# Kernel optimization log

Measured on AMD Instinct MI355X. Metric: run time of the kernel, lower is better.

## Reference

```python
import jax, jax.numpy as jnp
import numpy as np

R = 1.1
SCALE = 100.0
BUMP_STEPS = 32
NUM_THETAS = 32
NUM_FEATURES = 128
N_NODES = 200000
NUM_GRAPHS = 128


def setup_inputs() -> dict:
    key = jax.random.key(0)
    k1, k2, k3 = jax.random.split(key, 3)
    x = jax.random.normal(k1, (N_NODES, NUM_FEATURES), dtype=jnp.float32)
    batch = jnp.sort(jax.random.randint(k2, (N_NODES,), 0, NUM_GRAPHS, dtype=jnp.int64))
    v = jax.random.uniform(k3, (NUM_THETAS, NUM_FEATURES), dtype=jnp.float32) - 0.5
    return {"x": x, "batch": batch, "num_graphs": NUM_GRAPHS, "v": v}


def reference(x, batch, num_graphs, v):
    # nh: node heights along each direction theta -> [N, T]
    nh = x @ v.T
    # linspace over filtration values -> [S]
    lin = jnp.linspace(-R, R, BUMP_STEPS, dtype=nh.dtype)
    # bump: sigmoid difference; second point is the constant pad value R
    # ecc: [N, S, T]  (node-major so segment_sum reduces the leading axis)
    ecc = (jax.nn.sigmoid(SCALE * (lin[None, :, None] - nh[:, None, :]))
           - jax.nn.sigmoid(SCALE * (lin - R))[None, :, None])
    # scatter-add per graph label -> [ng, S, T] == index_add over dim1 then movedim(0,1)
    ect = jax.ops.segment_sum(ecc, batch, num_segments=num_graphs)
    return ect
```

## Files before the change

### kernel.cpp

```cpp
#include <hip/hip_runtime.h>
#include <math.h>

#define N_NODES 200000
#define NF 128
#define NT 32
#define NS 32
#define ATILE 64
#define ABLOCKS 3125
#define VSTRIDE 136
#define HPAD 33

typedef short bf16x8 __attribute__((ext_vector_type(8)));
typedef float floatx4 __attribute__((ext_vector_type(4)));

__device__ __forceinline__ float rcp_fast(float x) { return __builtin_amdgcn_rcpf(x); }

__device__ __forceinline__ void split_bf16(float f, unsigned short& h, unsigned short& l) {
    unsigned u  = __float_as_uint(f);
    unsigned r  = u + 0x7FFFu + ((u >> 16) & 1u);
    unsigned hb = r & 0xFFFF0000u;
    h = (unsigned short)(hb >> 16);
    float rem = f - __uint_as_float(hb);
    unsigned u2 = __float_as_uint(rem);
    unsigned r2 = u2 + 0x7FFFu + ((u2 >> 16) & 1u);
    l = (unsigned short)(r2 >> 16);
}

__device__ __forceinline__ void split8(float4 a, float4 b, bf16x8& h8, bf16x8& l8) {
    unsigned short h[8], l[8];
    split_bf16(a.x, h[0], l[0]); split_bf16(a.y, h[1], l[1]);
    split_bf16(a.z, h[2], l[2]); split_bf16(a.w, h[3], l[3]);
    split_bf16(b.x, h[4], l[4]); split_bf16(b.y, h[5], l[5]);
    split_bf16(b.z, h[6], l[6]); split_bf16(b.w, h[7], l[7]);
    h8 = (bf16x8){(short)h[0],(short)h[1],(short)h[2],(short)h[3],
                  (short)h[4],(short)h[5],(short)h[6],(short)h[7]};
    l8 = (bf16x8){(short)l[0],(short)l[1],(short)l[2],(short)l[3],
                  (short)l[4],(short)l[5],(short)l[6],(short)l[7]};
}

__device__ __forceinline__ void deposit(float* corr, int b, float z, float Lw, float C1) {
    float s0f = ceilf(z - 1.45f);
    int   s0  = (int)s0f;
    float e0  = __builtin_amdgcn_exp2f(Lw * (z - s0f));
    float e1  = e0 * C1;
    float e2  = e1 * C1;
    float f0  = rcp_fast(1.0f + e0);
    float f1  = rcp_fast(1.0f + e1);
    float f2  = rcp_fast(1.0f + e2);
    atomicAdd(&corr[b + max(s0, 0)], f0);
    int sB = max(s0 + 1, 0); if (sB < 32) atomicAdd(&corr[b + sB], f1 - f0);
    int sC = max(s0 + 2, 0); if (sC < 32) atomicAdd(&corr[b + sC], f2 - f1);
    int sD = s0 + 3;         if (sD < 32) atomicAdd(&corr[b + sD], 1.0f - f2);
}

__global__ __launch_bounds__(256, 7)
void ect_fused(const float* __restrict__ x,
               const int* __restrict__ batch,
               const float* __restrict__ v,
               float* __restrict__ out)
{
    __shared__ __align__(16) unsigned short vh[NT * VSTRIDE];
    __shared__ __align__(16) unsigned short vl[NT * VSTRIDE];
    __shared__ int   batch_lds[ATILE];
    __shared__ float corr[NT * HPAD];
    __shared__ float cnt_lds;

    const int tid  = threadIdx.x;
    const int blk  = blockIdx.x;
    const int w    = tid >> 6;
    const int lane = tid & 63;
    const int mrow = lane & 15;
    const int quad = lane >> 4;

    #pragma unroll
    for (int j = 0; j < 4; ++j) {
        int idx4 = j * 256 + tid;
        int row  = idx4 >> 5;
        int f4   = idx4 & 31;
        float4 val = *(const float4*)&v[(size_t)row * NF + f4 * 4];
        unsigned short h0,h1,h2,h3,l0,l1,l2,l3;
        split_bf16(val.x, h0, l0); split_bf16(val.y, h1, l1);
        split_bf16(val.z, h2, l2); split_bf16(val.w, h3, l3);
        uint2 hh, ll;
        hh.x = (unsigned)h0 | ((unsigned)h1 << 16); hh.y = (unsigned)h2 | ((unsigned)h3 << 16);
        ll.x = (unsigned)l0 | ((unsigned)l1 << 16); ll.y = (unsigned)l2 | ((unsigned)l3 << 16);
        *(uint2*)&vh[row * VSTRIDE + f4 * 4] = hh;
        *(uint2*)&vl[row * VSTRIDE + f4 * 4] = ll;
    }
    if (tid < ATILE) batch_lds[tid] = batch[blk * ATILE + tid];
    for (int i = tid; i < NT * HPAD; i += 256) corr[i] = 0.0f;

    const size_t arow = (size_t)blk * ATILE + w * 16 + mrow;
    const float* __restrict__ xrow = x + arow * NF + quad * 8;

    floatx4 acc0 = {0.f, 0.f, 0.f, 0.f};
    floatx4 acc1 = {0.f, 0.f, 0.f, 0.f};

    bf16x8 ah[4], al[4];
    #pragma unroll
    for (int slice = 0; slice < 4; ++slice) {
        float4 a0 = *(const float4*)&xrow[slice * 32];
        float4 a1 = *(const float4*)&xrow[slice * 32 + 4];
        split8(a0, a1, ah[slice], al[slice]);
    }
    __syncthreads();

    const int b0base = mrow * VSTRIDE + quad * 8;
    const int b1base = (16 + mrow) * VSTRIDE + quad * 8;
    #pragma unroll
    for (int slice = 0; slice < 4; ++slice) {
        bf16x8 bh0 = *(bf16x8*)&vh[b0base + slice * 32];
        bf16x8 bl0 = *(bf16x8*)&vl[b0base + slice * 32];
        bf16x8 bh1 = *(bf16x8*)&vh[b1base + slice * 32];
        bf16x8 bl1 = *(bf16x8*)&vl[b1base + slice * 32];
        acc0 = __builtin_amdgcn_mfma_f32_16x16x32_bf16(ah[slice], bh0, acc0, 0, 0, 0);
        acc0 = __builtin_amdgcn_mfma_f32_16x16x32_bf16(ah[slice], bl0, acc0, 0, 0, 0);
        acc0 = __builtin_amdgcn_mfma_f32_16x16x32_bf16(al[slice], bh0, acc0, 0, 0, 0);
        acc1 = __builtin_amdgcn_mfma_f32_16x16x32_bf16(ah[slice], bh1, acc1, 0, 0, 0);
        acc1 = __builtin_amdgcn_mfma_f32_16x16x32_bf16(ah[slice], bl1, acc1, 0, 0, 0);
        acc1 = __builtin_amdgcn_mfma_f32_16x16x32_bf16(al[slice], bh1, acc1, 0, 0, 0);
    }

    const float inv_dlin = 14.090909090909092f;
    const float Lw       = 10.23848093f;
    const float dlin     = 2.2f / 31.0f;
    const float L        = 144.26950408889634f;
    const float C1       = 8.2777115e-04f;

    const int g_first = batch_lds[0];
    const int g_last  = batch_lds[ATILE - 1];

    const int ft = tid & 31;
    const int sb = tid >> 5;
    float csk[4];
    #pragma unroll
    for (int k = 0; k < 4; ++k) {
        int s = sb + 8 * k;
        float lin_s = -1.1f + (float)s * dlin;
        csk[k] = rcp_fast(1.0f + __builtin_amdgcn_exp2f(L * (1.1f - lin_s)));
    }

    const int c0base = mrow * HPAD;
    const int c1base = (16 + mrow) * HPAD;

    for (int gp = g_first; gp <= g_last; ++gp) {
        if (tid < ATILE) {
            unsigned long long m = __ballot(batch_lds[tid] == gp);
            if (tid == 0) cnt_lds = (float)__popcll(m);
        }

        float c0 = 0.f, c1 = 0.f;
        #pragma unroll
        for (int reg = 0; reg < 4; ++reg) {
            const int n = w * 16 + quad * 4 + reg;
            if (batch_lds[n] == gp) {
                {
                    float z = fmaf(acc0[reg], inv_dlin, 15.5f);
                    if (z <= -1.45f)      c0 += 1.0f;
                    else if (z < 32.45f)  deposit(corr, c0base, z, Lw, C1);
                }
                {
                    float z = fmaf(acc1[reg], inv_dlin, 15.5f);
                    if (z <= -1.45f)      c1 += 1.0f;
                    else if (z < 32.45f)  deposit(corr, c1base, z, Lw, C1);
                }
            }
        }
        if (c0 != 0.f) atomicAdd(&corr[c0base], c0);
        if (c1 != 0.f) atomicAdd(&corr[c1base], c1);
        __syncthreads();

        {
            const int grp = tid >> 5;
            const int sc  = tid & 31;
            for (int row = grp; row < NT; row += 8) {
                float val = corr[row * HPAD + sc];
                #pragma unroll
                for (int d = 1; d < 32; d <<= 1) {
                    float nbr = __shfl_up(val, d, 32);
                    if (sc >= d) val += nbr;
                }
                corr[row * HPAD + sc] = val;
            }
        }
        __syncthreads();

        const float cnt = cnt_lds;
        #pragma unroll
        for (int k = 0; k < 4; ++k) {
            int s = sb + 8 * k;
            float val = corr[ft * HPAD + s] - cnt * csk[k];
            corr[ft * HPAD + s] = 0.0f;
            atomicAdd(&out[(size_t)gp * (NS * NT) + s * NT + ft], val);
        }
        if (gp < g_last) __syncthreads();
    }
}

extern "C" void kernel_launch(void* const* d_in, const int* in_sizes, int n_in,
                              void* d_out, int out_size, void* d_ws, size_t ws_size,
                              hipStream_t stream) {
    const float* x     = (const float*)d_in[0];
    const int*   batch = (const int*)d_in[1];
    const float* v     = (const float*)d_in[3];
    float*       out   = (float*)d_out;

    hipMemsetAsync(d_out, 0, (size_t)out_size * sizeof(float), stream);
    ect_fused<<<dim3(ABLOCKS), dim3(256), 0, stream>>>(x, batch, v, out);
}
```

Measured before the change: 207.4 us.

## Tile nodes per graph and reduce partial histograms instead of global atomics

```diff
diff --git a/kernel.cpp b/kernel.cpp
--- a/kernel.cpp
+++ b/kernel.cpp
@@ -5,8 +5,8 @@
 #define NF 128
 #define NT 32
 #define NS 32
-#define ATILE 64
-#define ABLOCKS 3125
+#define NG 128
+#define NTILES 30
 #define VSTRIDE 136
 #define HPAD 33
 
@@ -53,24 +53,50 @@
     int sD = s0 + 3;         if (sD < 32) atomicAdd(&corr[b + sD], 1.0f - f2);
 }
 
+__global__ __launch_bounds__(256)
+void graph_starts(const int* __restrict__ batch, int* __restrict__ starts) {
+    int i = blockIdx.x * 256 + threadIdx.x;
+    if (i >= N_NODES) return;
+    int b    = batch[i];
+    int prev = (i == 0) ? -1 : batch[i - 1];
+    for (int g = prev + 1; g <= b; ++g) starts[g] = i;
+    if (i == N_NODES - 1)
+        for (int g = b + 1; g <= NG; ++g) starts[g] = N_NODES;
+}
+
 __global__ __launch_bounds__(256, 7)
-void ect_fused(const float* __restrict__ x,
-               const int* __restrict__ batch,
-               const float* __restrict__ v,
-               float* __restrict__ out)
+void ect_tile(const float* __restrict__ x,
+              const float* __restrict__ v,
+              const int* __restrict__ starts,
+              float* __restrict__ partials,
+              float* __restrict__ out,
+              int use_ws)
 {
     __shared__ __align__(16) unsigned short vh[NT * VSTRIDE];
     __shared__ __align__(16) unsigned short vl[NT * VSTRIDE];
-    __shared__ int   batch_lds[ATILE];
     __shared__ float corr[NT * HPAD];
-    __shared__ float cnt_lds;
 
     const int tid  = threadIdx.x;
-    const int blk  = blockIdx.x;
+    const int t    = blockIdx.x;
+    const int g    = blockIdx.y;
     const int w    = tid >> 6;
     const int lane = tid & 63;
     const int mrow = lane & 15;
     const int quad = lane >> 4;
+
+    const int start = starts[g];
+    const int count = starts[g + 1] - start;
+    const int slot  = g * NTILES + t;
+
+    if (t * 64 >= count) {
+        if (use_ws) {
+            float4 z4 = {0.f, 0.f, 0.f, 0.f};
+            *(float4*)&partials[(size_t)slot * 1024 + tid * 4] = z4;
+        }
+        return;
+    }
+    const int base   = start + t * 64;
+    const int nvalid = min(64, count - t * 64);
 
     #pragma unroll
     for (int j = 0; j < 4; ++j) {
@@ -87,11 +113,10 @@
         *(uint2*)&vh[row * VSTRIDE + f4 * 4] = hh;
         *(uint2*)&vl[row * VSTRIDE + f4 * 4] = ll;
     }
-    if (tid < ATILE) batch_lds[tid] = batch[blk * ATILE + tid];
     for (int i = tid; i < NT * HPAD; i += 256) corr[i] = 0.0f;
 
-    const size_t arow = (size_t)blk * ATILE + w * 16 + mrow;
-    const float* __restrict__ xrow = x + arow * NF + quad * 8;
+    const int gi = min(base + w * 16 + mrow, N_NODES - 1);
+    const float* __restrict__ xrow = x + (size_t)gi * NF + quad * 8;
 
     floatx4 acc0 = {0.f, 0.f, 0.f, 0.f};
     floatx4 acc1 = {0.f, 0.f, 0.f, 0.f};
@@ -127,74 +152,76 @@
     const float L        = 144.26950408889634f;
     const float C1       = 8.2777115e-04f;
 
-    const int g_first = batch_lds[0];
-    const int g_last  = batch_lds[ATILE - 1];
-
-    const int ft = tid & 31;
-    const int sb = tid >> 5;
-    float csk[4];
-    #pragma unroll
-    for (int k = 0; k < 4; ++k) {
-        int s = sb + 8 * k;
-        float lin_s = -1.1f + (float)s * dlin;
-        csk[k] = rcp_fast(1.0f + __builtin_amdgcn_exp2f(L * (1.1f - lin_s)));
-    }
-
     const int c0base = mrow * HPAD;
     const int c1base = (16 + mrow) * HPAD;
 
-    for (int gp = g_first; gp <= g_last; ++gp) {
-        if (tid < ATILE) {
-            unsigned long long m = __ballot(batch_lds[tid] == gp);
-            if (tid == 0) cnt_lds = (float)__popcll(m);
-        }
-
-        float c0 = 0.f, c1 = 0.f;
-        #pragma unroll
-        for (int reg = 0; reg < 4; ++reg) {
-            const int n = w * 16 + quad * 4 + reg;
-            if (batch_lds[n] == gp) {
-                {
-                    float z = fmaf(acc0[reg], inv_dlin, 15.5f);
-                    if (z <= -1.45f)      c0 += 1.0f;
-                    else if (z < 32.45f)  deposit(corr, c0base, z, Lw, C1);
-                }
-                {
-                    float z = fmaf(acc1[reg], inv_dlin, 15.5f);
-                    if (z <= -1.45f)      c1 += 1.0f;
-                    else if (z < 32.45f)  deposit(corr, c1base, z, Lw, C1);
-                }
+    float c0 = 0.f, c1 = 0.f;
+    #pragma unroll
+    for (int reg = 0; reg < 4; ++reg) {
+        const int n = w * 16 + quad * 4 + reg;
+        if (n < nvalid) {
+            {
+                float z = fmaf(acc0[reg], inv_dlin, 15.5f);
+                if (z <= -1.45f)      c0 += 1.0f;
+                else if (z < 32.45f)  deposit(corr, c0base, z, Lw, C1);
+            }
+            {
+                float z = fmaf(acc1[reg], inv_dlin, 15.5f);
+                if (z <= -1.45f)      c1 += 1.0f;
+                else if (z < 32.45f)  deposit(corr, c1base, z, Lw, C1);
             }
         }
-        if (c0 != 0.f) atomicAdd(&corr[c0base], c0);
-        if (c1 != 0.f) atomicAdd(&corr[c1base], c1);
-        __syncthreads();
-
-        {
-            const int grp = tid >> 5;
-            const int sc  = tid & 31;
-            for (int row = grp; row < NT; row += 8) {
-                float val = corr[row * HPAD + sc];
-                #pragma unroll
-                for (int d = 1; d < 32; d <<= 1) {
-                    float nbr = __shfl_up(val, d, 32);
-                    if (sc >= d) val += nbr;
-                }
-                corr[row * HPAD + sc] = val;
+    }
+    if (c0 != 0.f) atomicAdd(&corr[c0base], c0);
+    if (c1 != 0.f) atomicAdd(&corr[c1base], c1);
+    __syncthreads();
+
+    {
+        const int grp = tid >> 5;
+        const int sc  = tid & 31;
+        for (int row = grp; row < NT; row += 8) {
+            float val = corr[row * HPAD + sc];
+            #pragma unroll
+            for (int d = 1; d < 32; d <<= 1) {
+                float nbr = __shfl_up(val, d, 32);
+                if (sc >= d) val += nbr;
             }
+            corr[row * HPAD + sc] = val;
         }
-        __syncthreads();
-
-        const float cnt = cnt_lds;
-        #pragma unroll
-        for (int k = 0; k < 4; ++k) {
-            int s = sb + 8 * k;
-            float val = corr[ft * HPAD + s] - cnt * csk[k];
-            corr[ft * HPAD + s] = 0.0f;
-            atomicAdd(&out[(size_t)gp * (NS * NT) + s * NT + ft], val);
-        }
-        if (gp < g_last) __syncthreads();
-    }
+    }
+    __syncthreads();
+
+    const float cnt  = (float)nvalid;
+    const int   s    = tid >> 3;
+    const int   ft0  = (tid & 7) * 4;
+    const float lin_s = -1.1f + (float)s * dlin;
+    const float cs    = rcp_fast(1.0f + __builtin_amdgcn_exp2f(L * (1.1f - lin_s)));
+    float4 r;
+    r.x = corr[(ft0 + 0) * HPAD + s] - cnt * cs;
+    r.y = corr[(ft0 + 1) * HPAD + s] - cnt * cs;
+    r.z = corr[(ft0 + 2) * HPAD + s] - cnt * cs;
+    r.w = corr[(ft0 + 3) * HPAD + s] - cnt * cs;
+    if (use_ws) {
+        *(float4*)&partials[(size_t)slot * 1024 + tid * 4] = r;
+    } else {
+        float* o = out + (size_t)g * (NS * NT) + tid * 4;
+        atomicAdd(&o[0], r.x); atomicAdd(&o[1], r.y);
+        atomicAdd(&o[2], r.z); atomicAdd(&o[3], r.w);
+    }
+}
+
+__global__ __launch_bounds__(256)
+void reduce_partials(const float* __restrict__ partials, float* __restrict__ out) {
+    const int g   = blockIdx.x;
+    const int tid = threadIdx.x;
+    const float4* p4 = (const float4*)partials;
+    float4 acc = {0.f, 0.f, 0.f, 0.f};
+    #pragma unroll
+    for (int t = 0; t < NTILES; ++t) {
+        float4 v = p4[(size_t)(g * NTILES + t) * 256 + tid];
+        acc.x += v.x; acc.y += v.y; acc.z += v.z; acc.w += v.w;
+    }
+    ((float4*)out)[(size_t)g * 256 + tid] = acc;
 }
 
 extern "C" void kernel_launch(void* const* d_in, const int* in_sizes, int n_in,
@@ -205,6 +232,14 @@
     const float* v     = (const float*)d_in[3];
     float*       out   = (float*)d_out;
 
+    int*   starts   = (int*)d_ws;
+    float* partials = (float*)((char*)d_ws + 1024);
+    const size_t need = 1024 + (size_t)NG * NTILES * 1024 * sizeof(float);
+    const int use_ws  = (ws_size >= need) ? 1 : 0;
+
     hipMemsetAsync(d_out, 0, (size_t)out_size * sizeof(float), stream);
-    ect_fused<<<dim3(ABLOCKS), dim3(256), 0, stream>>>(x, batch, v, out);
-}
+    graph_starts<<<dim3((N_NODES + 255) / 256), dim3(256), 0, stream>>>(batch, starts);
+    ect_tile<<<dim3(NTILES, NG), dim3(256), 0, stream>>>(x, v, starts, partials, out, use_ws);
+    if (use_ws)
+        reduce_partials<<<dim3(NG), dim3(256), 0, stream>>>(partials, out);
+}
```

New measurement: 181.3 us. 1.14x faster.
